# Performance work log

Measured on AMD Instinct MI355X. Metric: run time of the kernel, lower is better.

## Reference

```python
import jax, jax.numpy as jnp
import numpy as np

VOL = (64, 64, 64)
EPS = 1e-06
B, T, C, H, W = 2, 128, 1, 256, 256


def setup_inputs() -> dict:
    key = jax.random.key(0)
    k1, k2, k3, k4 = jax.random.split(key, 4)
    slices = jax.random.normal(k1, (B, T, C, H, W), dtype=jnp.float32)
    # translation coords at half-integer grid positions inside the volume so
    # min distance to any voxel is ~0.866 (keeps exp(1/d) finite in fp32)
    trans_xyz = jax.random.randint(k2, (B, T, 3), 0, VOL[0]).astype(jnp.float32) + 0.5
    rot = jax.random.normal(k3, (B, T, 3), dtype=jnp.float32)
    transforms = jnp.concatenate([trans_xyz, rot], axis=-1)  # [B, T, 6]
    slice_indices = jax.random.randint(k4, (B, T), 0, T)
    return {"slices": slices, "transforms": transforms, "slice_indices": slice_indices}


def reference(slices, transforms, slice_indices):
    vx, vy, vz = VOL
    V = vx * vy * vz
    b, t, c, h, w = slices.shape
    # gather selected transforms [B,T,D] and slices [B,T,C,H,W]
    sel_t = jnp.take_along_axis(transforms, slice_indices[:, :, None], axis=1)
    sel_s = jnp.take_along_axis(
        slices, slice_indices[:, :, None, None, None], axis=1)
    # voxel grid coords [V,3] (meshgrid 'ij')
    gx, gy, gz = jnp.meshgrid(jnp.arange(vx), jnp.arange(vy), jnp.arange(vz), indexing="ij")
    grid = jnp.stack([gx, gy, gz], axis=-1).reshape(V, 3).astype(slices.dtype)
    slice_coords = sel_t[..., :3]  # [B,T,3]
    # distances [B,T,V]
    diff = grid[None, None, :, :] - slice_coords[:, :, None, :]
    dist = jnp.sqrt(jnp.sum(diff * diff, axis=-1))
    wgt = jnp.exp(1.0 / (dist + EPS))
    wgt = wgt / jnp.sum(wgt, axis=1, keepdims=True)  # normalize over slices T
    # (W^T @ I).mean over HW == W^T @ mean(I) by linearity
    intensity_mean = sel_s.reshape(b, t, -1).mean(axis=-1)  # [B,T]
    recon = jnp.einsum("btv,bt->bv", wgt, intensity_mean)  # [B,V]
    return recon.reshape(b, 1, vx, vy, vz)
```

## Files before the change

kernel.cpp:

```cpp
#include <hip/hip_runtime.h>

#define VCNT 262144
#define NB 2
#define NT 128
#define HWPIX 65536
#define LN2 0.69314718055994531f

typedef float f32x2 __attribute__((ext_vector_type(2)));

static __device__ __forceinline__ float fast_exp2(float x) {
#if __has_builtin(__builtin_amdgcn_exp2f)
    return __builtin_amdgcn_exp2f(x);
#else
    float r; asm("v_exp_f32 %0, %1" : "=v"(r) : "v"(x)); return r;
#endif
}
static __device__ __forceinline__ float fast_rsq(float x) {
#if __has_builtin(__builtin_amdgcn_rsqf)
    return __builtin_amdgcn_rsqf(x);
#else
    float r; asm("v_rsq_f32 %0, %1" : "=v"(r) : "v"(x)); return r;
#endif
}

__global__ __launch_bounds__(256) void slice_partial_kernel(
    const float* __restrict__ slices, const int* __restrict__ sidx,
    float* __restrict__ partials)
{
    const int s   = blockIdx.x >> 3;
    const int b   = s >> 7;
    const int tsl = s & 127;

    __shared__ int needed;
    if (threadIdx.x == 0) needed = 0;
    __syncthreads();
    if (threadIdx.x < NT && sidx[(b << 7) + threadIdx.x] == tsl) needed = 1;
    __syncthreads();
    if (!needed) return;

    const int j = blockIdx.x & 7;
    const float4* p = (const float4*)(slices + (size_t)s * HWPIX) + j * 2048;

    float acc = 0.0f;
#pragma unroll
    for (int i = 0; i < 8; ++i) {
        float4 v = p[i * 256 + threadIdx.x];
        acc += (v.x + v.y) + (v.z + v.w);
    }
#pragma unroll
    for (int off = 32; off > 0; off >>= 1)
        acc += __shfl_down(acc, off, 64);

    __shared__ float ws[4];
    const int lane = threadIdx.x & 63;
    const int wid  = threadIdx.x >> 6;
    if (lane == 0) ws[wid] = acc;
    __syncthreads();
    if (threadIdx.x == 0)
        partials[blockIdx.x] = (ws[0] + ws[1]) + (ws[2] + ws[3]);
}

__global__ __launch_bounds__(256) void recon_kernel(
    const float* __restrict__ transforms,
    const int*   __restrict__ sidx,
    const float* __restrict__ partials,
    float*       __restrict__ out)
{
    __shared__ float4 ct[NT];
    __shared__ float  kk[NT];
    __shared__ int    wcnt[2];
    __shared__ int    ncnt;

    const int tid = threadIdx.x;
    const int b   = blockIdx.x >> 9;
    const int v0  = ((blockIdx.x & 511) << 9) + (tid << 1);

    int u = 0, k = 0, first = 0;
    if (tid < NT) {
        u = sidx[(b << 7) + tid];
        first = 1;
        for (int j = 0; j < NT; ++j) {
            const int m = (sidx[(b << 7) + j] == u) ? 1 : 0;
            k += m;
            if (m && j < tid) first = 0;
        }
    }
    const unsigned long long mask = __ballot(first);
    const int lane = tid & 63;
    const int wid  = tid >> 6;
    if (tid < NT && lane == 0) wcnt[wid] = (int)__popcll(mask);
    __syncthreads();
    if (first) {
        const int pos = (int)__popcll(mask & ((1ull << lane) - 1ull))
                      + (wid ? wcnt[0] : 0);
        const float* tr = transforms + (size_t)((b << 7) + u) * 6;
        const float* pp = partials   + (size_t)((b << 7) + u) * 8;
        float m = 0.0f;
#pragma unroll
        for (int i = 0; i < 8; ++i) m += pp[i];
        m *= (1.0f / (float)HWPIX);
        const float fk = (float)k;
        ct[pos] = make_float4(tr[0] * LN2, tr[1] * LN2, tr[2] * LN2, fk * m);
        kk[pos] = fk;
    }
    if (tid == 0) ncnt = wcnt[0] + wcnt[1];
    __syncthreads();
    const int n = ncnt;

    const float fx = (float)(v0 >> 12) * LN2;
    const float fy = (float)((v0 >> 6) & 63) * LN2;
    const float fz = (float)(v0 & 63) * LN2;

    const f32x2 fx2 = {fx, fx};
    const f32x2 fy2 = {fy, fy};
    const f32x2 fz2 = {fz, fz + LN2};

    f32x2 wsum = {0.0f, 0.0f};
    f32x2 acc  = {0.0f, 0.0f};

#pragma unroll 4
    for (int t = 0; t < n; ++t) {
        const float4 c  = ct[t];
        const float  kf = kk[t];
        f32x2 dx = fx2 - c.x;
        f32x2 dy = fy2 - c.y;
        f32x2 dz = fz2 - c.z;
        f32x2 d2 = dx * dx + dy * dy + dz * dz;
        f32x2 w;
        w.x = fast_exp2(fast_rsq(d2.x));
        w.y = fast_exp2(fast_rsq(d2.y));
        wsum += w * kf;
        acc  += w * c.w;
    }

    float2 o;
    o.x = acc.x / wsum.x;
    o.y = acc.y / wsum.y;
    *(float2*)(out + (size_t)b * VCNT + v0) = o;
}

extern "C" void kernel_launch(void* const* d_in, const int* in_sizes, int n_in,
                              void* d_out, int out_size, void* d_ws, size_t ws_size,
                              hipStream_t stream)
{
    const float* slices     = (const float*)d_in[0];
    const float* transforms = (const float*)d_in[1];
    const int*   sidx       = (const int*)d_in[2];
    float* out      = (float*)d_out;
    float* partials = (float*)d_ws;

    slice_partial_kernel<<<NB * NT * 8, 256, 0, stream>>>(slices, sidx, partials);
    recon_kernel<<<NB * VCNT / 512, 256, 0, stream>>>(transforms, sidx, partials, out);
}
```

Before: 29.56 us.

## Compute four voxels per thread and count slice duplicates with shared atomics

Each thread now computes four consecutive z-voxels instead of two. The dx/dy partial distance and the shared-memory loads of slice parameters are reused across all four, and results go out as a single float4 store. The grid is halved to match. The O(T^2) duplicate-index scan in the prologue is replaced by a shared-memory atomic histogram over slice indices, which also orders unique slices by index. The trade-off is more registers per thread and fewer blocks, which may reduce occupancy and latency hiding.

```diff
diff --git a/kernel.cpp b/kernel.cpp
--- a/kernel.cpp
+++ b/kernel.cpp
@@ -4,7 +4,8 @@
 #define NB 2
 #define NT 128
 #define HWPIX 65536
-#define LN2 0.69314718055994531f
+#define LN2  0.69314718055994531f
+#define LN2X2 1.38629436111989062f
 
 typedef float f32x2 __attribute__((ext_vector_type(2)));
 
@@ -68,33 +69,31 @@
 {
     __shared__ float4 ct[NT];
     __shared__ float  kk[NT];
+    __shared__ int    cnt[NT];
     __shared__ int    wcnt[2];
     __shared__ int    ncnt;
 
     const int tid = threadIdx.x;
-    const int b   = blockIdx.x >> 9;
-    const int v0  = ((blockIdx.x & 511) << 9) + (tid << 1);
+    const int b   = blockIdx.x >> 8;
+    const int v0  = ((blockIdx.x & 255) << 10) + (tid << 2);
 
-    int u = 0, k = 0, first = 0;
-    if (tid < NT) {
-        u = sidx[(b << 7) + tid];
-        first = 1;
-        for (int j = 0; j < NT; ++j) {
-            const int m = (sidx[(b << 7) + j] == u) ? 1 : 0;
-            k += m;
-            if (m && j < tid) first = 0;
-        }
-    }
-    const unsigned long long mask = __ballot(first);
+    if (tid < NT) cnt[tid] = 0;
+    __syncthreads();
+    if (tid < NT) atomicAdd(&cnt[sidx[(b << 7) + tid]], 1);
+    __syncthreads();
+
+    const int  k      = (tid < NT) ? cnt[tid] : 0;
+    const bool neededf = (k > 0);
+    const unsigned long long mask = __ballot(neededf);
     const int lane = tid & 63;
     const int wid  = tid >> 6;
     if (tid < NT && lane == 0) wcnt[wid] = (int)__popcll(mask);
     __syncthreads();
-    if (first) {
+    if (neededf) {
         const int pos = (int)__popcll(mask & ((1ull << lane) - 1ull))
                       + (wid ? wcnt[0] : 0);
-        const float* tr = transforms + (size_t)((b << 7) + u) * 6;
-        const float* pp = partials   + (size_t)((b << 7) + u) * 8;
+        const float* tr = transforms + (size_t)((b << 7) + tid) * 6;
+        const float* pp = partials   + (size_t)((b << 7) + tid) * 8;
         float m = 0.0f;
 #pragma unroll
         for (int i = 0; i < 8; ++i) m += pp[i];
@@ -107,36 +106,44 @@
     __syncthreads();
     const int n = ncnt;
 
-    const float fx = (float)(v0 >> 12) * LN2;
-    const float fy = (float)((v0 >> 6) & 63) * LN2;
-    const float fz = (float)(v0 & 63) * LN2;
+    const float fx  = (float)(v0 >> 12) * LN2;
+    const float fy  = (float)((v0 >> 6) & 63) * LN2;
+    const float fz0 = (float)(v0 & 63) * LN2;
+    const f32x2 fzp = {fz0, fz0 + LN2};
 
-    const f32x2 fx2 = {fx, fx};
-    const f32x2 fy2 = {fy, fy};
-    const f32x2 fz2 = {fz, fz + LN2};
+    f32x2 wsumA = {0.0f, 0.0f}, accA = {0.0f, 0.0f};
+    f32x2 wsumB = {0.0f, 0.0f}, accB = {0.0f, 0.0f};
 
-    f32x2 wsum = {0.0f, 0.0f};
-    f32x2 acc  = {0.0f, 0.0f};
-
-#pragma unroll 4
+#pragma unroll 2
     for (int t = 0; t < n; ++t) {
         const float4 c  = ct[t];
         const float  kf = kk[t];
-        f32x2 dx = fx2 - c.x;
-        f32x2 dy = fy2 - c.y;
-        f32x2 dz = fz2 - c.z;
-        f32x2 d2 = dx * dx + dy * dy + dz * dz;
-        f32x2 w;
-        w.x = fast_exp2(fast_rsq(d2.x));
-        w.y = fast_exp2(fast_rsq(d2.y));
-        wsum += w * kf;
-        acc  += w * c.w;
+        const float dx = fx - c.x;
+        const float dy = fy - c.y;
+        const float base = fmaf(dy, dy, dx * dx);
+        f32x2 dz0 = fzp - c.z;
+        f32x2 d2a = dz0 * dz0 + base;
+        f32x2 dz1 = dz0 + LN2X2;
+        f32x2 d2b = dz1 * dz1 + base;
+
+        f32x2 wA, wB;
+        wA.x = fast_exp2(fast_rsq(d2a.x));
+        wA.y = fast_exp2(fast_rsq(d2a.y));
+        wB.x = fast_exp2(fast_rsq(d2b.x));
+        wB.y = fast_exp2(fast_rsq(d2b.y));
+
+        wsumA += wA * kf;
+        accA  += wA * c.w;
+        wsumB += wB * kf;
+        accB  += wB * c.w;
     }
 
-    float2 o;
-    o.x = acc.x / wsum.x;
-    o.y = acc.y / wsum.y;
-    *(float2*)(out + (size_t)b * VCNT + v0) = o;
+    float4 o;
+    o.x = accA.x / wsumA.x;
+    o.y = accA.y / wsumA.y;
+    o.z = accB.x / wsumB.x;
+    o.w = accB.y / wsumB.y;
+    *(float4*)(out + (size_t)b * VCNT + v0) = o;
 }
 
 extern "C" void kernel_launch(void* const* d_in, const int* in_sizes, int n_in,
@@ -150,5 +157,5 @@
     float* partials = (float*)d_ws;
 
     slice_partial_kernel<<<NB * NT * 8, 256, 0, stream>>>(slices, sidx, partials);
-    recon_kernel<<<NB * VCNT / 512, 256, 0, stream>>>(transforms, sidx, partials, out);
+    recon_kernel<<<NB * VCNT / 1024, 256, 0, stream>>>(transforms, sidx, partials, out);
 }
```

New measurement: 26.64 us. 9.9% less time.

## Broadcast slice params via readlane, histogram counts with LDS atomics, split reduction finer

Applied to the files above, without the earlier changes.

Each thread now holds one unique slice's parameters in registers, and the inner loop broadcasts them with readlane, so it no longer reads LDS on every iteration. The O(T^2) duplicate scan becomes a shared-memory atomic histogram. The partial-sum kernel is split into 16 blocks per slice instead of 8, and the recon kernel combines those partials with float4 loads. The distance computation reuses the shared dx^2+dy^2 term for both voxels and uses explicit FMAs, at the cost of more SGPR/readlane traffic and a duplicated loop body.

```diff
diff --git a/kernel.cpp b/kernel.cpp
--- a/kernel.cpp
+++ b/kernel.cpp
@@ -22,12 +22,15 @@
     float r; asm("v_rsq_f32 %0, %1" : "=v"(r) : "v"(x)); return r;
 #endif
 }
+static __device__ __forceinline__ float rl_f(float v, int l) {
+    return __uint_as_float(__builtin_amdgcn_readlane(__float_as_uint(v), l));
+}
 
 __global__ __launch_bounds__(256) void slice_partial_kernel(
     const float* __restrict__ slices, const int* __restrict__ sidx,
     float* __restrict__ partials)
 {
-    const int s   = blockIdx.x >> 3;
+    const int s   = blockIdx.x >> 4;
     const int b   = s >> 7;
     const int tsl = s & 127;
 
@@ -38,15 +41,18 @@
     __syncthreads();
     if (!needed) return;
 
-    const int j = blockIdx.x & 7;
-    const float4* p = (const float4*)(slices + (size_t)s * HWPIX) + j * 2048;
+    const int j = blockIdx.x & 15;
+    const float4* p = (const float4*)(slices + (size_t)s * HWPIX) + j * 1024;
 
-    float acc = 0.0f;
-#pragma unroll
-    for (int i = 0; i < 8; ++i) {
-        float4 v = p[i * 256 + threadIdx.x];
-        acc += (v.x + v.y) + (v.z + v.w);
-    }
+    const float4 a0 = p[threadIdx.x];
+    const float4 a1 = p[256 + threadIdx.x];
+    const float4 a2 = p[512 + threadIdx.x];
+    const float4 a3 = p[768 + threadIdx.x];
+    float acc = ((a0.x + a0.y) + (a0.z + a0.w))
+              + ((a1.x + a1.y) + (a1.z + a1.w))
+              + ((a2.x + a2.y) + (a2.z + a2.w))
+              + ((a3.x + a3.y) + (a3.z + a3.w));
+
 #pragma unroll
     for (int off = 32; off > 0; off >>= 1)
         acc += __shfl_down(acc, off, 64);
@@ -68,36 +74,35 @@
 {
     __shared__ float4 ct[NT];
     __shared__ float  kk[NT];
+    __shared__ int    cnt[NT];
     __shared__ int    wcnt[2];
     __shared__ int    ncnt;
 
-    const int tid = threadIdx.x;
-    const int b   = blockIdx.x >> 9;
-    const int v0  = ((blockIdx.x & 511) << 9) + (tid << 1);
-
-    int u = 0, k = 0, first = 0;
-    if (tid < NT) {
-        u = sidx[(b << 7) + tid];
-        first = 1;
-        for (int j = 0; j < NT; ++j) {
-            const int m = (sidx[(b << 7) + j] == u) ? 1 : 0;
-            k += m;
-            if (m && j < tid) first = 0;
-        }
-    }
-    const unsigned long long mask = __ballot(first);
+    const int tid  = threadIdx.x;
     const int lane = tid & 63;
     const int wid  = tid >> 6;
+    const int b    = blockIdx.x >> 9;
+
+    if (tid < NT) cnt[tid] = 0;
+    __syncthreads();
+    if (tid < NT) atomicAdd(&cnt[sidx[(b << 7) + tid]], 1);
+    __syncthreads();
+
+    const int  k       = (tid < NT) ? cnt[tid] : 0;
+    const bool neededf = (k > 0);
+    const unsigned long long mask = __ballot(neededf);
     if (tid < NT && lane == 0) wcnt[wid] = (int)__popcll(mask);
     __syncthreads();
-    if (first) {
+    if (neededf) {
         const int pos = (int)__popcll(mask & ((1ull << lane) - 1ull))
                       + (wid ? wcnt[0] : 0);
-        const float* tr = transforms + (size_t)((b << 7) + u) * 6;
-        const float* pp = partials   + (size_t)((b << 7) + u) * 8;
-        float m = 0.0f;
-#pragma unroll
-        for (int i = 0; i < 8; ++i) m += pp[i];
+        const float* tr = transforms + (size_t)((b << 7) + tid) * 6;
+        const float4* pp = (const float4*)(partials + (size_t)((b << 7) + tid) * 16);
+        const float4 q0 = pp[0], q1 = pp[1], q2 = pp[2], q3 = pp[3];
+        float m = ((q0.x + q0.y) + (q0.z + q0.w))
+                + ((q1.x + q1.y) + (q1.z + q1.w))
+                + ((q2.x + q2.y) + (q2.z + q2.w))
+                + ((q3.x + q3.y) + (q3.z + q3.w));
         m *= (1.0f / (float)HWPIX);
         const float fk = (float)k;
         ct[pos] = make_float4(tr[0] * LN2, tr[1] * LN2, tr[2] * LN2, fk * m);
@@ -105,32 +110,53 @@
     }
     if (tid == 0) ncnt = wcnt[0] + wcnt[1];
     __syncthreads();
-    const int n = ncnt;
+    const int n = __builtin_amdgcn_readfirstlane(ncnt);
 
+    const float4 cA = ct[lane];
+    const float  kA = kk[lane];
+    const float4 cB = ct[64 + lane];
+    const float  kB = kk[64 + lane];
+
+    const int v0 = ((blockIdx.x & 511) << 9) + (tid << 1);
     const float fx = (float)(v0 >> 12) * LN2;
     const float fy = (float)((v0 >> 6) & 63) * LN2;
     const float fz = (float)(v0 & 63) * LN2;
-
-    const f32x2 fx2 = {fx, fx};
-    const f32x2 fy2 = {fy, fy};
-    const f32x2 fz2 = {fz, fz + LN2};
+    const f32x2 fzp = {fz, fz + LN2};
 
     f32x2 wsum = {0.0f, 0.0f};
     f32x2 acc  = {0.0f, 0.0f};
 
+    const int nA = (n < 64) ? n : 64;
 #pragma unroll 4
-    for (int t = 0; t < n; ++t) {
-        const float4 c  = ct[t];
-        const float  kf = kk[t];
-        f32x2 dx = fx2 - c.x;
-        f32x2 dy = fy2 - c.y;
-        f32x2 dz = fz2 - c.z;
-        f32x2 d2 = dx * dx + dy * dy + dz * dz;
-        f32x2 w;
+    for (int t = 0; t < nA; ++t) {
+        const float cx = rl_f(cA.x, t), cy = rl_f(cA.y, t), cz = rl_f(cA.z, t);
+        const float cw = rl_f(cA.w, t), ck = rl_f(kA, t);
+        const float dx = fx - cx;
+        const float dy = fy - cy;
+        const float base = fmaf(dy, dy, dx * dx);
+        f32x2 dz, d2, w;
+        dz.x = fzp.x - cz;            dz.y = fzp.y - cz;
+        d2.x = fmaf(dz.x, dz.x, base); d2.y = fmaf(dz.y, dz.y, base);
         w.x = fast_exp2(fast_rsq(d2.x));
         w.y = fast_exp2(fast_rsq(d2.y));
-        wsum += w * kf;
-        acc  += w * c.w;
+        wsum.x = fmaf(w.x, ck, wsum.x);  wsum.y = fmaf(w.y, ck, wsum.y);
+        acc.x  = fmaf(w.x, cw, acc.x);   acc.y  = fmaf(w.y, cw, acc.y);
+    }
+#pragma unroll 4
+    for (int t = 64; t < n; ++t) {
+        const int l = t - 64;
+        const float cx = rl_f(cB.x, l), cy = rl_f(cB.y, l), cz = rl_f(cB.z, l);
+        const float cw = rl_f(cB.w, l), ck = rl_f(kB, l);
+        const float dx = fx - cx;
+        const float dy = fy - cy;
+        const float base = fmaf(dy, dy, dx * dx);
+        f32x2 dz, d2, w;
+        dz.x = fzp.x - cz;            dz.y = fzp.y - cz;
+        d2.x = fmaf(dz.x, dz.x, base); d2.y = fmaf(dz.y, dz.y, base);
+        w.x = fast_exp2(fast_rsq(d2.x));
+        w.y = fast_exp2(fast_rsq(d2.y));
+        wsum.x = fmaf(w.x, ck, wsum.x);  wsum.y = fmaf(w.y, ck, wsum.y);
+        acc.x  = fmaf(w.x, cw, acc.x);   acc.y  = fmaf(w.y, cw, acc.y);
     }
 
     float2 o;
@@ -149,6 +175,6 @@
     float* out      = (float*)d_out;
     float* partials = (float*)d_ws;
 
-    slice_partial_kernel<<<NB * NT * 8, 256, 0, stream>>>(slices, sidx, partials);
+    slice_partial_kernel<<<NB * NT * 16, 256, 0, stream>>>(slices, sidx, partials);
     recon_kernel<<<NB * VCNT / 512, 256, 0, stream>>>(transforms, sidx, partials, out);
 }
```

Result: slower. 32.22 us (+9.0%).
